# Performance work log

Measured on AMD Instinct MI355X. Metric: run time of the kernel, lower is better.

Reference implementation:

```python
import jax, jax.numpy as jnp
import numpy as np

B, S, D, H, DK, DV, W = 2, 8192, 1024, 16, 64, 64, 128


def setup_inputs() -> dict:
    key = jax.random.key(0)
    ks = jax.random.split(key, 5)
    scale = 0.02
    x = jax.random.normal(ks[0], (B, S, D), jnp.float32)
    Wq = jax.random.normal(ks[1], (D, H * DK), jnp.float32) * scale
    Wk = jax.random.normal(ks[2], (D, H * DK), jnp.float32) * scale
    Wv = jax.random.normal(ks[3], (D, H * DV), jnp.float32) * scale
    Wo = jax.random.normal(ks[4], (H * DV, D), jnp.float32) * scale
    return {"x": x, "Wq": Wq, "Wk": Wk, "Wv": Wv, "Wo": Wo, "window_size": W}


def _sliding_window_attn(x, Wq, Wk, Wv, Wo, window_size):
    b, s, d = x.shape
    dk = Wq.shape[1] // H
    dv = Wv.shape[1] // H
    Bq = window_size            # block size == band half-width
    nb = s // Bq                # number of query blocks

    # projections -> [B, H, S, dh]
    q = (x @ Wq).reshape(b, s, H, dk).transpose(0, 2, 1, 3)
    k = (x @ Wk).reshape(b, s, H, dk).transpose(0, 2, 1, 3)
    v = (x @ Wv).reshape(b, s, H, dv).transpose(0, 2, 1, 3)

    qb = q.reshape(b, H, nb, Bq, dk)

    # pad keys/values by one block on each side, gather 3-block local context
    kpad = jnp.pad(k, ((0, 0), (0, 0), (Bq, Bq), (0, 0)))
    vpad = jnp.pad(v, ((0, 0), (0, 0), (Bq, Bq), (0, 0)))
    kb = kpad.reshape(b, H, nb + 2, Bq, dk)
    vb = vpad.reshape(b, H, nb + 2, Bq, dv)
    kctx = jnp.concatenate([kb[:, :, :-2], kb[:, :, 1:-1], kb[:, :, 2:]], axis=3)  # [B,H,nb,3Bq,dk]
    vctx = jnp.concatenate([vb[:, :, :-2], vb[:, :, 1:-1], vb[:, :, 2:]], axis=3)  # [B,H,nb,3Bq,dv]

    scores = jnp.einsum("bhnqd,bhnkd->bhnqk", qb, kctx) / jnp.sqrt(jnp.asarray(dk, x.dtype))

    # banded mask: query global idx i = n*Bq + q_loc; key global idx j = (n-1)*Bq + k_loc
    q_loc = jnp.arange(Bq)[:, None]                 # [Bq,1]
    k_rel = jnp.arange(3 * Bq)[None, :] - Bq        # [1,3Bq], offset of j relative to block start
    band = jnp.abs(k_rel - q_loc) <= window_size    # [Bq,3Bq]
    j_global = jnp.arange(nb)[:, None, None] * Bq + k_rel[None]  # [nb,1,3Bq]
    valid = (j_global >= 0) & (j_global < s)
    mask = band[None] & valid                       # [nb,Bq,3Bq]

    neg = jnp.asarray(-1e9, scores.dtype)
    scores = jnp.where(mask[None, None], scores, neg)
    attn = jax.nn.softmax(scores, axis=-1)

    ctx = jnp.einsum("bhnqk,bhnkd->bhnqd", attn, vctx)           # [B,H,nb,Bq,dv]
    ctx = ctx.reshape(b, H, s, dv).transpose(0, 2, 1, 3).reshape(b, s, H * dv)
    return ctx @ Wo


def reference(x, Wq, Wk, Wv, Wo, window_size):
    return _sliding_window_attn(x, Wq, Wk, Wv, Wo, window_size)
```

## Files before the change

kernel.cpp:

```cpp
#include <hip/hip_runtime.h>


typedef __bf16 bf16_t;
typedef bf16_t bf16x8 __attribute__((ext_vector_type(8)));
typedef bf16_t bf16x4 __attribute__((ext_vector_type(4)));
typedef float f32x4 __attribute__((ext_vector_type(4)));

#define CEXP 0.18033688011112042f

__device__ __forceinline__ f32x4 mfma16(bf16x8 a, bf16x8 b, f32x4 c) {
  return __builtin_amdgcn_mfma_f32_16x16x32_bf16(a, b, c, 0, 0, 0);
}

#define GLL16(gptr, lptr)                                                     \
  __builtin_amdgcn_global_load_lds(                                           \
      (__attribute__((address_space(1))) void*)(gptr),                        \
      (__attribute__((address_space(3))) void*)(lptr), 16, 0, 0)

__global__ __launch_bounds__(256) void prep(const float* __restrict__ x,
                                            const float* __restrict__ W0,
                                            const float* __restrict__ W1,
                                            const float* __restrict__ W2,
                                            const float* __restrict__ W3,
                                            bf16_t* __restrict__ xb,
                                            bf16_t* T0, bf16_t* T1,
                                            bf16_t* T2, bf16_t* T3) {
  __shared__ float tile[32][33];
  const int t = threadIdx.x;
  if (blockIdx.x < 8192) {
    int i = blockIdx.x * 256 + t;
    f32x4 a = *(const f32x4*)&x[(size_t)i * 8];
    f32x4 b = *(const f32x4*)&x[(size_t)i * 8 + 4];
    bf16x8 o;
#pragma unroll
    for (int j = 0; j < 4; ++j) { o[j] = (bf16_t)a[j]; o[4 + j] = (bf16_t)b[j]; }
    *(bf16x8*)&xb[(size_t)i * 8] = o;
    return;
  }
  int wb = blockIdx.x - 8192;
  int z = wb >> 10, rem = wb & 1023;
  int bx = rem & 31, by = rem >> 5;
  const float* W; bf16_t* T;
  switch (z) {
    case 0: W = W0; T = T0; break;
    case 1: W = W1; T = T1; break;
    case 2: W = W2; T = T2; break;
    default: W = W3; T = T3; break;
  }
  const float s = (z == 0) ? CEXP : 1.0f;
  int tx = t & 31, ty = t >> 5;
  int xc = bx * 32 + tx;
  int y0 = by * 32;
#pragma unroll
  for (int i = ty; i < 32; i += 8) tile[i][tx] = W[(size_t)(y0 + i) * 1024 + xc];
  __syncthreads();
  int xo = y0 + tx;
  int yo = bx * 32;
#pragma unroll
  for (int i = ty; i < 32; i += 8)
    T[(size_t)(yo + i) * 1024 + xo] = (bf16_t)(tile[tx][i] * s);
}

__device__ __forceinline__ void gemm256_loop(const bf16_t* __restrict__ A,
                                             const bf16_t* __restrict__ Bt,
                                             int m0, int n0,
                                             bf16_t (*As)[8192],
                                             bf16_t (*Bs)[8192],
                                             f32x4 acc[8][4]) {
  const int K = 1024, NT = 32;
  const int t = threadIdx.x, l = t & 63, w = t >> 6;
  const int fr = l & 15, quad = l >> 4;
  const int wm = w >> 2, wn = w & 3;
  const int srow = w * 16 + (l >> 2);
  const int scol = ((l & 3) ^ ((l >> 3) & 3)) << 3;
  const bf16_t* Asrc = A + (size_t)(m0 + srow) * K + scol;
  const bf16_t* Bsrc = Bt + (size_t)(n0 + srow) * K + scol;
  const size_t cstep = (size_t)128 * K;
  const int sdst = w * 512 + l * 8;
  const int rdoff = fr * 32 + ((quad ^ ((fr >> 1) & 3)) << 3);
  const int abase = wm * 4096 + rdoff;
  const int bbase = wn * 2048 + rdoff;

#pragma unroll
  for (int tt = 0; tt < 2; ++tt) {
    GLL16(Asrc + tt * 32, &As[tt][sdst]);
    GLL16(Asrc + cstep + tt * 32, &As[tt][4096 + sdst]);
    GLL16(Bsrc + tt * 32, &Bs[tt][sdst]);
    GLL16(Bsrc + cstep + tt * 32, &Bs[tt][4096 + sdst]);
  }
  asm volatile("s_waitcnt vmcnt(4)" ::: "memory");
  __builtin_amdgcn_s_barrier();

  bf16x8 bq[4], bq2[4], afA[4], afB[4];
#pragma unroll
  for (int j = 0; j < 4; ++j) bq[j] = *(const bf16x8*)&Bs[0][bbase + j * 512];
#pragma unroll
  for (int i = 0; i < 4; ++i) afA[i] = *(const bf16x8*)&As[0][abase + i * 512];

#pragma unroll 4
  for (int tk = 0; tk < NT; ++tk) {
    const bf16_t* Ap = As[tk & 3];
    __builtin_amdgcn_s_setprio(1);
#pragma unroll
    for (int i = 0; i < 4; ++i) afB[i] = *(const bf16x8*)&Ap[abase + (4 + i) * 512];
#pragma unroll
    for (int i = 0; i < 4; ++i)
#pragma unroll
      for (int j = 0; j < 4; ++j) acc[i][j] = mfma16(afA[i], bq[j], acc[i][j]);
    __builtin_amdgcn_s_setprio(0);
    if (tk + 2 < NT) {
      const int s2 = (tk + 2) & 3;
      GLL16(Asrc + (tk + 2) * 32, &As[s2][sdst]);
      GLL16(Asrc + cstep + (tk + 2) * 32, &As[s2][4096 + sdst]);
      GLL16(Bsrc + (tk + 2) * 32, &Bs[s2][sdst]);
      GLL16(Bsrc + cstep + (tk + 2) * 32, &Bs[s2][4096 + sdst]);
      asm volatile("s_waitcnt vmcnt(4)" ::: "memory");
    } else {
      asm volatile("s_waitcnt vmcnt(0)" ::: "memory");
    }
    __builtin_amdgcn_s_barrier();
    __builtin_amdgcn_s_setprio(1);
    if (tk + 1 < NT) {
      const bf16_t* An = As[(tk + 1) & 3];
      const bf16_t* Bn = Bs[(tk + 1) & 3];
#pragma unroll
      for (int j = 0; j < 4; ++j) bq2[j] = *(const bf16x8*)&Bn[bbase + j * 512];
#pragma unroll
      for (int i = 0; i < 4; ++i) afA[i] = *(const bf16x8*)&An[abase + i * 512];
    }
#pragma unroll
    for (int i = 0; i < 4; ++i)
#pragma unroll
      for (int j = 0; j < 4; ++j) acc[4 + i][j] = mfma16(afB[i], bq[j], acc[4 + i][j]);
    __builtin_amdgcn_s_setprio(0);
    __builtin_amdgcn_s_barrier();
#pragma unroll
    for (int j = 0; j < 4; ++j) bq[j] = bq2[j];
  }
}

__global__ __launch_bounds__(512, 2) void gemm_qkv(const bf16_t* __restrict__ A,
                                                   const bf16_t* __restrict__ Bt,
                                                   bf16_t* __restrict__ qh,
                                                   bf16_t* __restrict__ kh,
                                                   bf16_t* __restrict__ vT2) {
  __shared__ bf16_t As[4][8192];
  __shared__ bf16_t Bs[4][8192];
  const int id = blockIdx.y * 12 + blockIdx.x;
  const int swz = (id & 7) * 96 + (id >> 3);
  const int m0 = (swz / 12) << 8, n0 = (swz % 12) << 8;

  f32x4 acc[8][4] = {};
  gemm256_loop(A, Bt, m0, n0, As, Bs, acc);

  const int t = threadIdx.x, l = t & 63, w = t >> 6;
  const int fr = l & 15, quad = l >> 4;
  const int wm = w >> 2, wn = w & 3;
  const int colbase = n0 + wn * 64;
  if (colbase < 2048) {
    bf16_t* dst = (colbase < 1024) ? qh : kh;
    const int cb = colbase & 1023;
#pragma unroll
    for (int i = 0; i < 8; ++i)
#pragma unroll
      for (int j = 0; j < 4; ++j) {
        int col = cb + j * 16 + fr;
        int h = col >> 6, dk = col & 63;
#pragma unroll
        for (int r = 0; r < 4; ++r) {
          int cm = m0 + wm * 128 + i * 16 + quad * 4 + r;
          int b = cm >> 13, s = cm & 8191;
          dst[((((size_t)(b * 16 + h) << 13) | s) << 6) | dk] = (bf16_t)acc[i][j][r];
        }
      }
  } else {
    const int cb = colbase - 2048;
#pragma unroll
    for (int i = 0; i < 8; ++i) {
      int s0 = m0 + wm * 128 + i * 16;
      int b = s0 >> 13, sblk = (s0 & 8191) >> 4;
#pragma unroll
      for (int j = 0; j < 4; ++j) {
        int col = cb + j * 16;
        int h = col >> 6, dv = (col & 63) + fr;
        bf16x4 pk;
#pragma unroll
        for (int r = 0; r < 4; ++r) pk[r] = (bf16_t)acc[i][j][r];
        *(bf16x4*)&vT2[((size_t)(b * 16 + h) * 512 + sblk) * 1024 + dv * 16 + quad * 4] = pk;
      }
    }
  }
}

__global__ __launch_bounds__(512, 2) void gemm_bt(const bf16_t* __restrict__ A,
                                                  const bf16_t* __restrict__ Bt,
                                                  float* __restrict__ Cf) {
  __shared__ bf16_t As[4][8192];
  __shared__ bf16_t Bs[4][8192];
  const int id = blockIdx.y * 4 + blockIdx.x;
  const int swz = (id & 7) * 32 + (id >> 3);
  const int m0 = (swz >> 2) << 8, n0 = (swz & 3) << 8;

  f32x4 acc[8][4] = {};
  gemm256_loop(A, Bt, m0, n0, As, Bs, acc);

  const int t = threadIdx.x, l = t & 63, w = t >> 6;
  const int fr = l & 15, quad = l >> 4;
  const int wm = w >> 2, wn = w & 3;
#pragma unroll
  for (int i = 0; i < 8; ++i)
#pragma unroll
    for (int j = 0; j < 4; ++j)
#pragma unroll
      for (int r = 0; r < 4; ++r) {
        int cm = m0 + wm * 128 + i * 16 + quad * 4 + r;
        int cn = n0 + wn * 64 + j * 16 + fr;
        Cf[(size_t)cm * 1024 + cn] = acc[i][j][r];
      }
}

#define SKK 72
#define SVS 136
#define PST 136

__global__ __launch_bounds__(256, 3) void swa(const bf16_t* __restrict__ qh,
                                              const bf16_t* __restrict__ kh,
                                              const bf16_t* __restrict__ vT2,
                                              bf16_t* __restrict__ ctx) {
  __shared__ bf16_t Ks[128 * SKK];
  __shared__ bf16_t Vs[64 * SVS];
  __shared__ bf16_t PsT[4][16 * PST];

  const int t = threadIdx.x, lane = t & 63, w = t >> 6;
  const int L = (blockIdx.z * 16 + blockIdx.y) * 64 + blockIdx.x;
  const int swz = (L & 7) * 256 + (L >> 3);
  const int n = swz & 63, bhid = swz >> 6;
  const int h = bhid & 15, b = bhid >> 4;
  const int fr = lane & 15, quad = lane >> 4, fk = quad << 3;
  const size_t bh = (size_t)(b * 16 + h);

  bf16x8 aq[2][2];
  {
    const size_t qbase = (bh * 8192 + n * 128 + w * 32) * 64;
#pragma unroll
    for (int qt = 0; qt < 2; ++qt)
#pragma unroll
      for (int ks = 0; ks < 2; ++ks)
        aq[qt][ks] = *(const bf16x8*)&qh[qbase + (size_t)(qt * 16 + fr) * 64 + ks * 32 + fk];
  }

  bf16x8 ones;
#pragma unroll
  for (int j = 0; j < 8; ++j) ones[j] = (bf16_t)1.0f;

  bf16x8 kr[4], vr[4];
  auto loadKV = [&](int kn) {
#pragma unroll
    for (int it = 0; it < 4; ++it) {
      int c = it * 256 + t;
      kr[it] = *(const bf16x8*)&kh[(bh * 8192 + kn * 128 + (c >> 3)) * 64 + ((c & 7) << 3)];
      int sb = c >> 7, dv = (c & 127) >> 1, sh = c & 1;
      vr[it] = *(const bf16x8*)&vT2[(bh * 512 + kn * 8 + sb) * 1024 + dv * 16 + sh * 8];
    }
  };

  const int cbeg = (n == 0) ? 1 : 0;
  const int cend = (n == 63) ? 1 : 2;
  loadKV(n + cbeg - 1);

  f32x4 ls[2] = {};
  f32x4 o[2][4] = {};

  for (int ch = cbeg; ch <= cend; ++ch) {
    __syncthreads();
#pragma unroll
    for (int it = 0; it < 4; ++it) {
      int c = it * 256 + t;
      *(bf16x8*)&Ks[(c >> 3) * SKK + ((c & 7) << 3)] = kr[it];
      int sb = c >> 7, dv = (c & 127) >> 1, sh = c & 1;
      *(bf16x8*)&Vs[dv * SVS + sb * 16 + sh * 8] = vr[it];
    }
    __syncthreads();
    if (ch < cend) loadKV(n + ch);

#pragma unroll
    for (int qt = 0; qt < 2; ++qt) {
      const int lo = (ch == 0) ? 2 * w + qt : 0;
      const int hi = (ch == 2) ? 2 * w + qt : 7;

      f32x4 st[8];
      __builtin_amdgcn_s_setprio(1);
#pragma unroll
      for (int kt = 0; kt < 8; ++kt) {
        if (kt < lo || kt > hi) continue;
        bf16x8 k0 = *(const bf16x8*)&Ks[(kt * 16 + fr) * SKK + fk];
        bf16x8 k1 = *(const bf16x8*)&Ks[(kt * 16 + fr) * SKK + 32 + fk];
        st[kt] = mfma16(k1, aq[qt][1], mfma16(k0, aq[qt][0], (f32x4){0.f, 0.f, 0.f, 0.f}));
      }
      __builtin_amdgcn_s_setprio(0);

#pragma unroll
      for (int kt = 0; kt < 8; ++kt) {
        if (kt < lo || kt > hi) continue;
        const bool dL = (ch == 0) && (kt == lo);
        const bool dR = (ch == 2) && (kt == hi);
        bf16x4 pk;
#pragma unroll
        for (int r = 0; r < 4; ++r) {
          float p = exp2f(st[kt][r]);
          int kl = quad * 4 + r;
          if (dL) p = (kl >= fr) ? p : 0.f;
          if (dR) p = (kl <= fr) ? p : 0.f;
          pk[r] = (bf16_t)p;
        }
        *(bf16x4*)&PsT[w][fr * PST + kt * 16 + quad * 4] = pk;
      }
      if ((ch == 0) && (lo & 1)) {
        bf16x4 zz; zz[0] = zz[1] = zz[2] = zz[3] = (bf16_t)0.f;
        *(bf16x4*)&PsT[w][fr * PST + (lo - 1) * 16 + quad * 4] = zz;
      }
      if ((ch == 2) && !(hi & 1)) {
        bf16x4 zz; zz[0] = zz[1] = zz[2] = zz[3] = (bf16_t)0.f;
        *(bf16x4*)&PsT[w][fr * PST + (hi + 1) * 16 + quad * 4] = zz;
      }

      const int pl = lo >> 1, ph = hi >> 1;
      __builtin_amdgcn_s_setprio(1);
#pragma unroll
      for (int ks = 0; ks < 4; ++ks) {
        if (ks < pl || ks > ph) continue;
        bf16x8 pa = *(const bf16x8*)&PsT[w][fr * PST + ks * 32 + fk];
        ls[qt] = mfma16(pa, ones, ls[qt]);
#pragma unroll
        for (int dt = 0; dt < 4; ++dt) {
          bf16x8 bv = *(const bf16x8*)&Vs[(dt * 16 + fr) * SVS + ks * 32 + fk];
          o[qt][dt] = mfma16(pa, bv, o[qt][dt]);
        }
      }
      __builtin_amdgcn_s_setprio(0);
    }
  }

#pragma unroll
  for (int qt = 0; qt < 2; ++qt) {
    f32x4 rl;
#pragma unroll
    for (int r = 0; r < 4; ++r) rl[r] = __builtin_amdgcn_rcpf(ls[qt][r]);
#pragma unroll
    for (int dt = 0; dt < 4; ++dt)
#pragma unroll
      for (int r = 0; r < 4; ++r) {
        float ov = o[qt][dt][r] * rl[r];
        int srow = n * 128 + w * 32 + qt * 16 + quad * 4 + r;
        ctx[((size_t)b * 8192 + srow) * 1024 + h * 64 + dt * 16 + fr] = (bf16_t)ov;
      }
  }
}

extern "C" void kernel_launch(void* const* d_in, const int* in_sizes, int n_in,
                              void* d_out, int out_size, void* d_ws, size_t ws_size,
                              hipStream_t stream) {
  const float* x  = (const float*)d_in[0];
  const float* Wq = (const float*)d_in[1];
  const float* Wk = (const float*)d_in[2];
  const float* Wv = (const float*)d_in[3];
  const float* Wo = (const float*)d_in[4];
  float* out = (float*)d_out;

  char* p = (char*)d_ws;
  bf16_t* xb    = (bf16_t*)p; p += (size_t)16384 * 1024 * 2;
  bf16_t* WqkvT = (bf16_t*)p; p += (size_t)3 * 1024 * 1024 * 2;
  bf16_t* WoT   = (bf16_t*)p; p += (size_t)1024 * 1024 * 2;
  bf16_t* qhb   = (bf16_t*)p; p += (size_t)16384 * 1024 * 2;
  bf16_t* khb   = (bf16_t*)p; p += (size_t)16384 * 1024 * 2;
  bf16_t* vT2   = (bf16_t*)p; p += (size_t)16384 * 1024 * 2;
  bf16_t* ctx   = (bf16_t*)p; p += (size_t)16384 * 1024 * 2;

  prep<<<12288, 256, 0, stream>>>(x, Wq, Wk, Wv, Wo, xb, WqkvT,
                                  WqkvT + (size_t)1024 * 1024,
                                  WqkvT + (size_t)2 * 1024 * 1024, WoT);
  gemm_qkv<<<dim3(12, 64), 512, 0, stream>>>(xb, WqkvT, qhb, khb, vT2);
  swa<<<dim3(64, 16, 2), 256, 0, stream>>>(qhb, khb, vT2, ctx);
  gemm_bt<<<dim3(4, 64), 512, 0, stream>>>(ctx, WoT, out);
}
```

Before: 324.3 us.

## Switch GEMM main loop to BK=64 double-buffered LDS pipeline

Restructures the shared GEMM main loop from a 4-stage ring of 32-wide K tiles with split-half register prefetch to a 2-stage double buffer of 64-wide K tiles. It uses a new XOR swizzle over 8 column chunks and does one wait and barrier per tile. The aim is to halve the number of barriers and loop iterations and to issue all 64 MFMAs per tile in two bursts. In exchange, prefetch depth drops to one tile and LDS reads are no longer overlapped with MFMAs across iterations, so global-load latency may be exposed.

```diff
diff --git a/kernel.cpp b/kernel.cpp
--- a/kernel.cpp
+++ b/kernel.cpp
@@ -64,78 +64,70 @@
 __device__ __forceinline__ void gemm256_loop(const bf16_t* __restrict__ A,
                                              const bf16_t* __restrict__ Bt,
                                              int m0, int n0,
-                                             bf16_t (*As)[8192],
-                                             bf16_t (*Bs)[8192],
+                                             bf16_t (*As)[16384],
+                                             bf16_t (*Bs)[16384],
                                              f32x4 acc[8][4]) {
-  const int K = 1024, NT = 32;
+  const int K = 1024, NT = 16;
   const int t = threadIdx.x, l = t & 63, w = t >> 6;
   const int fr = l & 15, quad = l >> 4;
   const int wm = w >> 2, wn = w & 3;
-  const int srow = w * 16 + (l >> 2);
-  const int scol = ((l & 3) ^ ((l >> 3) & 3)) << 3;
+  const int srow = t >> 3;
+  const int scol = ((t & 7) ^ ((t >> 3) & 7)) << 3;
   const bf16_t* Asrc = A + (size_t)(m0 + srow) * K + scol;
   const bf16_t* Bsrc = Bt + (size_t)(n0 + srow) * K + scol;
-  const size_t cstep = (size_t)128 * K;
-  const int sdst = w * 512 + l * 8;
-  const int rdoff = fr * 32 + ((quad ^ ((fr >> 1) & 3)) << 3);
-  const int abase = wm * 4096 + rdoff;
-  const int bbase = wn * 2048 + rdoff;
-
-#pragma unroll
-  for (int tt = 0; tt < 2; ++tt) {
-    GLL16(Asrc + tt * 32, &As[tt][sdst]);
-    GLL16(Asrc + cstep + tt * 32, &As[tt][4096 + sdst]);
-    GLL16(Bsrc + tt * 32, &Bs[tt][sdst]);
-    GLL16(Bsrc + cstep + tt * 32, &Bs[tt][4096 + sdst]);
-  }
-  asm volatile("s_waitcnt vmcnt(4)" ::: "memory");
+  const size_t gstep = (size_t)64 * K;
+  const int sdst = t * 8;
+  const int arow = wm * 128 + fr;
+  const int brow = wn * 64 + fr;
+  const int fx = fr & 7;
+  const int c0 = (quad ^ fx) << 3;
+  const int c1 = ((4 + quad) ^ fx) << 3;
+
+#pragma unroll
+  for (int g = 0; g < 4; ++g) {
+    GLL16(Asrc + g * gstep, &As[0][g * 4096 + sdst]);
+    GLL16(Bsrc + g * gstep, &Bs[0][g * 4096 + sdst]);
+  }
+  asm volatile("s_waitcnt vmcnt(0)" ::: "memory");
   __builtin_amdgcn_s_barrier();
 
-  bf16x8 bq[4], bq2[4], afA[4], afB[4];
-#pragma unroll
-  for (int j = 0; j < 4; ++j) bq[j] = *(const bf16x8*)&Bs[0][bbase + j * 512];
-#pragma unroll
-  for (int i = 0; i < 4; ++i) afA[i] = *(const bf16x8*)&As[0][abase + i * 512];
-
-#pragma unroll 4
+#pragma unroll 2
   for (int tk = 0; tk < NT; ++tk) {
-    const bf16_t* Ap = As[tk & 3];
+    const int cs = tk & 1;
+    if (tk + 1 < NT) {
+      const bf16_t* An = Asrc + (size_t)(tk + 1) * 64;
+      const bf16_t* Bn = Bsrc + (size_t)(tk + 1) * 64;
+#pragma unroll
+      for (int g = 0; g < 4; ++g) {
+        GLL16(An + g * gstep, &As[cs ^ 1][g * 4096 + sdst]);
+        GLL16(Bn + g * gstep, &Bs[cs ^ 1][g * 4096 + sdst]);
+      }
+    }
+    const bf16_t* Ap = As[cs];
+    const bf16_t* Bp = Bs[cs];
+    bf16x8 af[8], bq[4];
+#pragma unroll
+    for (int i = 0; i < 8; ++i) af[i] = *(const bf16x8*)&Ap[(arow + i * 16) * 64 + c0];
+#pragma unroll
+    for (int j = 0; j < 4; ++j) bq[j] = *(const bf16x8*)&Bp[(brow + j * 16) * 64 + c0];
     __builtin_amdgcn_s_setprio(1);
 #pragma unroll
-    for (int i = 0; i < 4; ++i) afB[i] = *(const bf16x8*)&Ap[abase + (4 + i) * 512];
-#pragma unroll
-    for (int i = 0; i < 4; ++i)
-#pragma unroll
-      for (int j = 0; j < 4; ++j) acc[i][j] = mfma16(afA[i], bq[j], acc[i][j]);
+    for (int i = 0; i < 8; ++i)
+#pragma unroll
+      for (int j = 0; j < 4; ++j) acc[i][j] = mfma16(af[i], bq[j], acc[i][j]);
     __builtin_amdgcn_s_setprio(0);
-    if (tk + 2 < NT) {
-      const int s2 = (tk + 2) & 3;
-      GLL16(Asrc + (tk + 2) * 32, &As[s2][sdst]);
-      GLL16(Asrc + cstep + (tk + 2) * 32, &As[s2][4096 + sdst]);
-      GLL16(Bsrc + (tk + 2) * 32, &Bs[s2][sdst]);
-      GLL16(Bsrc + cstep + (tk + 2) * 32, &Bs[s2][4096 + sdst]);
-      asm volatile("s_waitcnt vmcnt(4)" ::: "memory");
-    } else {
-      asm volatile("s_waitcnt vmcnt(0)" ::: "memory");
-    }
+#pragma unroll
+    for (int i = 0; i < 8; ++i) af[i] = *(const bf16x8*)&Ap[(arow + i * 16) * 64 + c1];
+#pragma unroll
+    for (int j = 0; j < 4; ++j) bq[j] = *(const bf16x8*)&Bp[(brow + j * 16) * 64 + c1];
+    __builtin_amdgcn_s_setprio(1);
+#pragma unroll
+    for (int i = 0; i < 8; ++i)
+#pragma unroll
+      for (int j = 0; j < 4; ++j) acc[i][j] = mfma16(af[i], bq[j], acc[i][j]);
+    __builtin_amdgcn_s_setprio(0);
+    asm volatile("s_waitcnt vmcnt(0)" ::: "memory");
     __builtin_amdgcn_s_barrier();
-    __builtin_amdgcn_s_setprio(1);
-    if (tk + 1 < NT) {
-      const bf16_t* An = As[(tk + 1) & 3];
-      const bf16_t* Bn = Bs[(tk + 1) & 3];
-#pragma unroll
-      for (int j = 0; j < 4; ++j) bq2[j] = *(const bf16x8*)&Bn[bbase + j * 512];
-#pragma unroll
-      for (int i = 0; i < 4; ++i) afA[i] = *(const bf16x8*)&An[abase + i * 512];
-    }
-#pragma unroll
-    for (int i = 0; i < 4; ++i)
-#pragma unroll
-      for (int j = 0; j < 4; ++j) acc[4 + i][j] = mfma16(afB[i], bq[j], acc[4 + i][j]);
-    __builtin_amdgcn_s_setprio(0);
-    __builtin_amdgcn_s_barrier();
-#pragma unroll
-    for (int j = 0; j < 4; ++j) bq[j] = bq2[j];
   }
 }
 
@@ -144,8 +136,8 @@
                                                    bf16_t* __restrict__ qh,
                                                    bf16_t* __restrict__ kh,
                                                    bf16_t* __restrict__ vT2) {
-  __shared__ bf16_t As[4][8192];
-  __shared__ bf16_t Bs[4][8192];
+  __shared__ bf16_t As[2][16384];
+  __shared__ bf16_t Bs[2][16384];
   const int id = blockIdx.y * 12 + blockIdx.x;
   const int swz = (id & 7) * 96 + (id >> 3);
   const int m0 = (swz / 12) << 8, n0 = (swz % 12) << 8;
@@ -195,8 +187,8 @@
 __global__ __launch_bounds__(512, 2) void gemm_bt(const bf16_t* __restrict__ A,
                                                   const bf16_t* __restrict__ Bt,
                                                   float* __restrict__ Cf) {
-  __shared__ bf16_t As[4][8192];
-  __shared__ bf16_t Bs[4][8192];
+  __shared__ bf16_t As[2][16384];
+  __shared__ bf16_t Bs[2][16384];
   const int id = blockIdx.y * 4 + blockIdx.x;
   const int swz = (id & 7) * 32 + (id >> 3);
   const int m0 = (swz >> 2) << 8, n0 = (swz & 3) << 8;
```

After: 328.9 us. No clear change (+1.4%).
